# Kernel optimization log

Hardware: AMD Instinct MI355X
Metric: run time of the kernel (lower is better)

## Reference

```python
import jax, jax.numpy as jnp
import numpy as np

IMG = 32
CX = CY = IMG // 2
B = 65536


def setup_inputs() -> dict:
    key = jax.random.key(0)
    k1, k2, k3 = jax.random.split(key, 3)
    W = jax.random.normal(k1, (B, 16), dtype=jnp.float32)
    noise_randn = jax.random.normal(k2, (B, IMG, IMG), dtype=jnp.float32)
    noise_rand = jax.random.uniform(k3, (B, IMG, IMG), dtype=jnp.float32)
    return {"W": W, "noise_randn": noise_randn, "noise_rand": noise_rand}


def reference(W, noise_randn, noise_rand):
    H = IMG
    PI = jnp.float32(np.pi)
    ar = jnp.arange(H, dtype=jnp.float32)
    xx, yy = jnp.meshgrid(ar, ar, indexing="ij")  # (H, H)

    def c(k):  # per-sample scalar broadcast to (B,1,1)
        return W[:, k][:, None, None]

    r = jnp.sqrt((xx - CX) ** 2 + (yy - CY) ** 2)  # (H, H)

    # layer 0: clipped radial cone
    img = jnp.clip(c(0) * 5 - r, 0.0, 1.0)
    # layer 1: centered square (torch int(clamp(...).item()) == floor for positive vals)
    half = jnp.floor(jnp.clip(jnp.abs(c(1)) * 8, 2.0, 12.0))
    mask1 = ((xx >= CY - half) & (xx < CY + half) & (yy >= CX - half) & (yy < CX + half))
    img = img + 0.5 * mask1.astype(jnp.float32)
    # layers 2-4: sinusoids
    img = img + 0.5 * jnp.sin(c(2) * 10 * PI * xx / H)
    img = img + 0.5 * jnp.sin(c(3) * 10 * PI * yy / H)
    img = img + 0.5 * jnp.sin(c(4) * 5 * PI * (xx + yy) / (2 * H))
    # layer 5: warp
    img = img + 0.5 * jnp.sin((yy + c(5) * 10) * PI / H)
    # layer 6: bias
    img = img + c(6)
    # layer 7: gaussian blob; int() truncates toward zero
    bx = jnp.trunc(CX + c(7) * 5)
    by = jnp.trunc(CY + c(7) * 5)
    sigma = 4.0 + jnp.abs(c(7)) * 4.0
    img = img + jnp.exp(-((xx - bx) ** 2 + (yy - by) ** 2) / (2 * sigma ** 2))
    # layer 8: ring
    img = img + ((r - c(8) * 10) ** 2 < 10.0).astype(jnp.float32)
    # layer 9: checkerboard; cb_size = int(clamp(|w|*8+2, 2, 16)) -> floor
    cb = jnp.floor(jnp.clip(jnp.abs(c(9)) * 8 + 2, 2.0, 16.0))
    img = img + jnp.mod(jnp.floor(xx / cb) + jnp.floor(yy / cb), 2.0) * 0.3
    # layer 10: rotated line
    angle = c(10) * PI
    rot_line = jnp.cos(angle) * (xx - CX) + jnp.sin(angle) * (yy - CY)
    img = img + (jnp.abs(rot_line) < 3.0).astype(jnp.float32) * 0.6
    # layer 11: angular sinusoid
    theta = jnp.arctan2(yy - CY, xx - CX)
    img = img + 0.5 * jnp.sin(theta * c(11) * 5)
    # layers 12-13: noise (deterministic inputs replace randn_like/rand_like)
    img = img + noise_randn * 0.1 * c(12)
    img = img + (noise_rand - 0.5) * c(13) * 0.05
    # layer 14: contrast
    img = (img - 0.5) * (1.0 + c(14)) + 0.5
    # layer 15: conditional inversion
    img = jnp.where(c(15) > 0, 1.0 - img, img)
    # per-image min-max normalize
    mn = jnp.min(img, axis=(1, 2), keepdims=True)
    mx = jnp.max(img, axis=(1, 2), keepdims=True)
    img = (img - mn) / (mx - mn + 1e-8)
    return img[:, None, :, :]  # (B, 1, H, W)
```

## Files before the change

kernel.cpp:

```cpp
#include <hip/hip_runtime.h>
#include <math.h>

#define NB 65536
#define IMGD 32
#define NPIX 1024
#define PSTRIDE 20

__device__ float g_r[NPIX];
__device__ float g_th[NPIX];
__device__ float g_par[(size_t)NB * PSTRIDE];

__global__ void init_tables_kernel() {
    int p = threadIdx.x;
    int x = p >> 5, y = p & 31;
    float dx = (float)(x - 16), dy = (float)(y - 16);
    g_r[p] = sqrtf(dx * dx + dy * dy);
    g_th[p] = atan2f(dy, dx) * 0.79577471545947668f;
}

__global__ void init_params_kernel(const float* __restrict__ W) {
    int b = blockIdx.x * blockDim.x + threadIdx.x;
    if (b >= NB) return;
    const float* w = W + (size_t)b * 16;
    float* P = g_par + (size_t)b * PSTRIDE;

    float w0 = w[0], w1 = w[1], w2 = w[2], w3 = w[3], w4 = w[4], w5 = w[5],
          w6 = w[6], w7 = w[7], w8 = w[8], w9 = w[9], w10 = w[10], w11 = w[11],
          w12 = w[12], w13 = w[13], w14 = w[14], w15 = w[15];

    P[0] = w0 * 5.0f;
    float half = floorf(fminf(fmaxf(fabsf(w1) * 8.0f, 2.0f), 12.0f));
    P[1] = 16.0f - half;
    P[2] = 16.0f + half;
    P[3] = w2 * 0.15625f;
    P[4] = w3 * 0.15625f;
    P[5] = w4 * 0.0390625f;
    P[6] = w5 * 0.15625f;
    P[7] = w6;
    float t7 = __fadd_rn(16.0f, __fmul_rn(w7, 5.0f));
    P[8] = truncf(t7);
    float sg = 4.0f + fabsf(w7) * 4.0f;
    P[9] = -1.0f / (2.0f * sg * sg);
    P[10] = w8 * 10.0f;
    float cb = floorf(fminf(fmaxf(__fadd_rn(fabsf(w9) * 8.0f, 2.0f), 2.0f), 16.0f));
    P[11] = cb;
    P[12] = 1.0f / cb;
    float ang = __fmul_rn(w10, 3.14159265358979323846f);
    P[13] = (float)cos((double)ang);
    P[14] = (float)sin((double)ang);
    P[15] = w11;
    P[16] = w12 * 0.1f;
    P[17] = w13 * 0.05f;
    P[18] = 1.0f + w14;
    P[19] = w15;
}

__device__ __forceinline__ float hsin(float rev) {
    rev = rev - floorf(rev);
    return __builtin_amdgcn_sinf(rev);
}

__device__ __forceinline__ float fdivq(float xf, float cb, float rcb) {
    float q = floorf(xf * rcb);
    q += ((q + 1.0f) * cb <= xf) ? 1.0f : 0.0f;
    q -= ((q * cb) > xf) ? 1.0f : 0.0f;
    return q;
}

__global__ __launch_bounds__(256) void decode_kernel(
        const float* __restrict__ nrand,
        const float* __restrict__ nunif,
        float* __restrict__ out) {
    int b = blockIdx.x;
    int t = threadIdx.x;
    const float* P = g_par + (size_t)b * PSTRIDE;

    float a0  = P[0],  xlo = P[1],  xhi = P[2],  s2  = P[3],  s3 = P[4];
    float s4  = P[5],  s5o = P[6],  w6  = P[7],  bxy = P[8],  nk = P[9];
    float t8  = P[10], cb  = P[11], rcb = P[12], ca  = P[13], sa = P[14];
    float w11 = P[15], k12 = P[16], k13 = P[17], con = P[18], w15 = P[19];

    int p0 = t * 4;
    int x  = p0 >> 5;
    int y0 = p0 & 31;
    float xf = (float)x;

    float sin2  = 0.5f * hsin(s2 * xf);
    bool  mrow  = (xf >= xlo) && (xf < xhi);
    float dxb   = xf - bxy;
    float dxb2  = dxb * dxb;
    float qx    = fdivq(xf, cb, rcb);
    float rotx  = __fmul_rn(ca, xf - 16.0f);

    size_t base = (size_t)b * NPIX + (size_t)p0;
    float4 vr = *reinterpret_cast<const float4*>(nrand + base);
    float4 vu = *reinterpret_cast<const float4*>(nunif + base);
    float4 rr = *reinterpret_cast<const float4*>(g_r + p0);
    float4 tt = *reinterpret_cast<const float4*>(g_th + p0);

    const float* rrp = reinterpret_cast<const float*>(&rr);
    const float* ttp = reinterpret_cast<const float*>(&tt);
    const float* vrp = reinterpret_cast<const float*>(&vr);
    const float* vup = reinterpret_cast<const float*>(&vu);

    float img[4];
    float mn = 1e30f, mx = -1e30f;

#pragma unroll
    for (int j = 0; j < 4; ++j) {
        float yf = (float)(y0 + j);
        float r  = rrp[j];
        float th = ttp[j];

        float v = fminf(fmaxf(a0 - r, 0.0f), 1.0f);
        v += (mrow && (yf >= xlo) && (yf < xhi)) ? 0.5f : 0.0f;
        v += sin2;
        v += 0.5f * hsin(s3 * yf);
        v += 0.5f * hsin(s4 * (xf + yf));
        v += 0.5f * hsin(0.015625f * yf + s5o);
        v += w6;
        float dyb = yf - bxy;
        v += __expf((dxb2 + dyb * dyb) * nk);
        float dr = __fsub_rn(r, t8);
        v += (__fmul_rn(dr, dr) < 10.0f) ? 1.0f : 0.0f;
        float qy = fdivq(yf, cb, rcb);
        float s  = qx + qy;
        float par = s - 2.0f * floorf(s * 0.5f);
        v += par * 0.3f;
        float rot = __fadd_rn(rotx, __fmul_rn(sa, yf - 16.0f));
        v += (fabsf(rot) < 3.0f) ? 0.6f : 0.0f;
        v += 0.5f * hsin(th * w11);
        v += vrp[j] * k12;
        v += (vup[j] - 0.5f) * k13;
        v = (v - 0.5f) * con + 0.5f;
        v = (w15 > 0.0f) ? (1.0f - v) : v;

        img[j] = v;
        mn = fminf(mn, v);
        mx = fmaxf(mx, v);
    }

#pragma unroll
    for (int off = 32; off > 0; off >>= 1) {
        mn = fminf(mn, __shfl_xor(mn, off));
        mx = fmaxf(mx, __shfl_xor(mx, off));
    }
    __shared__ float smn[4], smx[4];
    int wid = t >> 6;
    if ((t & 63) == 0) { smn[wid] = mn; smx[wid] = mx; }
    __syncthreads();
    mn = fminf(fminf(smn[0], smn[1]), fminf(smn[2], smn[3]));
    mx = fmaxf(fmaxf(smx[0], smx[1]), fmaxf(smx[2], smx[3]));

    float inv = 1.0f / (mx - mn + 1e-8f);
    float4 o;
    o.x = (img[0] - mn) * inv;
    o.y = (img[1] - mn) * inv;
    o.z = (img[2] - mn) * inv;
    o.w = (img[3] - mn) * inv;
    *reinterpret_cast<float4*>(out + base) = o;
}

extern "C" void kernel_launch(void* const* d_in, const int* in_sizes, int n_in,
                              void* d_out, int out_size, void* d_ws, size_t ws_size,
                              hipStream_t stream) {
    const float* W  = (const float*)d_in[0];
    const float* nr = (const float*)d_in[1];
    const float* nu = (const float*)d_in[2];
    float* out = (float*)d_out;

    init_tables_kernel<<<1, 1024, 0, stream>>>();
    init_params_kernel<<<NB / 256, 256, 0, stream>>>(W);
    decode_kernel<<<NB, 256, 0, stream>>>(nr, nu, out);
}
```

Measured before the change: 172.1 us.

## Precompute separable row/column terms in shared tables and fold contrast/inversion into normalization

Splits the separable per-pixel terms (sinusoids, square mask, gaussian, checkerboard parity) into per-row and per-column shared-memory tables that the first 127 threads fill, plus a table for the x+y sinusoid. Each pixel then only does table lookups and FMAs. The contrast and conditional-inversion affine step is moved out of the per-pixel loop and folded algebraically into the final min-max normalization. This cuts transcendental work per pixel, at the cost of an extra __syncthreads, some shared-memory traffic, and a slightly different floating-point rounding order.

```diff
diff --git a/kernel.cpp b/kernel.cpp
--- a/kernel.cpp
+++ b/kernel.cpp
@@ -75,22 +75,51 @@
     int t = threadIdx.x;
     const float* P = g_par + (size_t)b * PSTRIDE;
 
-    float a0  = P[0],  xlo = P[1],  xhi = P[2],  s2  = P[3],  s3 = P[4];
+    float a0  = P[0],  lo  = P[1],  hi  = P[2],  s2  = P[3],  s3 = P[4];
     float s4  = P[5],  s5o = P[6],  w6  = P[7],  bxy = P[8],  nk = P[9];
     float t8  = P[10], cb  = P[11], rcb = P[12], ca  = P[13], sa = P[14];
     float w11 = P[15], k12 = P[16], k13 = P[17], con = P[18], w15 = P[19];
+
+    __shared__ float4 xt4[32];
+    __shared__ float4 yt4[32];
+    __shared__ float  stab[63];
+
+    if (t < 32) {
+        float xf = (float)t;
+        float qx = fdivq(xf, cb, rcb);
+        float px = qx - 2.0f * floorf(qx * 0.5f);
+        float d  = xf - bxy;
+        float4 e;
+        e.x = 0.5f * hsin(s2 * xf) + 0.3f * px;
+        e.y = (xf >= lo && xf < hi) ? 1.0f : 0.0f;
+        e.z = -0.6f * px;
+        e.w = __expf(d * d * nk);
+        xt4[t] = e;
+    } else if (t < 64) {
+        float yf = (float)(t - 32);
+        float qy = fdivq(yf, cb, rcb);
+        float py = qy - 2.0f * floorf(qy * 0.5f);
+        float d  = yf - bxy;
+        float4 e;
+        e.x = 0.5f * hsin(s3 * yf) + 0.5f * hsin(0.015625f * yf + s5o)
+              + 0.3f * py + w6;
+        e.y = (yf >= lo && yf < hi) ? 0.5f : 0.0f;
+        e.z = py;
+        e.w = __expf(d * d * nk);
+        yt4[t - 32] = e;
+    } else if (t < 127) {
+        int s = t - 64;
+        stab[s] = 0.5f * hsin(s4 * (float)s);
+    }
+    __syncthreads();
 
     int p0 = t * 4;
     int x  = p0 >> 5;
     int y0 = p0 & 31;
     float xf = (float)x;
 
-    float sin2  = 0.5f * hsin(s2 * xf);
-    bool  mrow  = (xf >= xlo) && (xf < xhi);
-    float dxb   = xf - bxy;
-    float dxb2  = dxb * dxb;
-    float qx    = fdivq(xf, cb, rcb);
-    float rotx  = __fmul_rn(ca, xf - 16.0f);
+    float4 X   = xt4[x];
+    float rotx = __fmul_rn(ca, xf - 16.0f);
 
     size_t base = (size_t)b * NPIX + (size_t)p0;
     float4 vr = *reinterpret_cast<const float4*>(nrand + base);
@@ -108,32 +137,24 @@
 
 #pragma unroll
     for (int j = 0; j < 4; ++j) {
-        float yf = (float)(y0 + j);
+        int   y  = y0 + j;
+        float yf = (float)y;
         float r  = rrp[j];
-        float th = ttp[j];
+        float4 Y = yt4[y];
 
         float v = fminf(fmaxf(a0 - r, 0.0f), 1.0f);
-        v += (mrow && (yf >= xlo) && (yf < xhi)) ? 0.5f : 0.0f;
-        v += sin2;
-        v += 0.5f * hsin(s3 * yf);
-        v += 0.5f * hsin(s4 * (xf + yf));
-        v += 0.5f * hsin(0.015625f * yf + s5o);
-        v += w6;
-        float dyb = yf - bxy;
-        v += __expf((dxb2 + dyb * dyb) * nk);
+        v += X.x + Y.x;
+        v = fmaf(X.y, Y.y, v);
+        v += stab[x + y];
+        v = fmaf(X.z, Y.z, v);
+        v = fmaf(X.w, Y.w, v);
         float dr = __fsub_rn(r, t8);
         v += (__fmul_rn(dr, dr) < 10.0f) ? 1.0f : 0.0f;
-        float qy = fdivq(yf, cb, rcb);
-        float s  = qx + qy;
-        float par = s - 2.0f * floorf(s * 0.5f);
-        v += par * 0.3f;
         float rot = __fadd_rn(rotx, __fmul_rn(sa, yf - 16.0f));
         v += (fabsf(rot) < 3.0f) ? 0.6f : 0.0f;
-        v += 0.5f * hsin(th * w11);
-        v += vrp[j] * k12;
-        v += (vup[j] - 0.5f) * k13;
-        v = (v - 0.5f) * con + 0.5f;
-        v = (w15 > 0.0f) ? (1.0f - v) : v;
+        v += 0.5f * hsin(ttp[j] * w11);
+        v = fmaf(vrp[j], k12, v);
+        v = fmaf(vup[j] - 0.5f, k13, v);
 
         img[j] = v;
         mn = fminf(mn, v);
@@ -152,12 +173,18 @@
     mn = fminf(fminf(smn[0], smn[1]), fminf(smn[2], smn[3]));
     mx = fmaxf(fmaxf(smx[0], smx[1]), fmaxf(smx[2], smx[3]));
 
-    float inv = 1.0f / (mx - mn + 1e-8f);
+    float ac    = fabsf(con);
+    float denom = fmaf(ac, mx - mn, 1e-8f);
+    float s     = ac / denom;
+    bool  eff   = (w15 > 0.0f) != (con < 0.0f);
+    float bse   = eff ? mx : mn;
+    float sgn   = eff ? -s : s;
+
     float4 o;
-    o.x = (img[0] - mn) * inv;
-    o.y = (img[1] - mn) * inv;
-    o.z = (img[2] - mn) * inv;
-    o.w = (img[3] - mn) * inv;
+    o.x = (img[0] - bse) * sgn;
+    o.y = (img[1] - bse) * sgn;
+    o.z = (img[2] - bse) * sgn;
+    o.w = (img[3] - bse) * sgn;
     *reinterpret_cast<float4*>(out + base) = o;
 }
 
```

Measured after the change: 148.7 us. 1.16x faster.
